# Performance work log

Measured on AMD Instinct MI355X. Metric: run time of the kernel, lower is better.

## Reference

```python
import jax, jax.numpy as jnp
import numpy as np

B, C, H, W = 128, 512, 14, 14
HEADS = 4
DH = C // HEADS  # 128
RH = RW = 7      # reduced KV grid (hardcoded 7x7 in source)
EPS = 1e-5
SCALE = DH ** -0.5


def _rel_pos_index():
    # replicates RelativePositionBias.__init__ index construction (h=w=7)
    coords = np.stack(np.meshgrid(np.arange(RH), np.arange(RW), indexing='ij'))
    cf = coords.reshape(2, -1)                       # [2,49]
    rc = cf[:, :, None] - cf[:, None, :]             # [2,49,49]
    rc = rc.transpose(1, 2, 0).copy()                # [49,49,2]
    rc[:, :, 0] += RH - 1
    rc[:, :, 1] += RW - 1
    rc[:, :, 0] *= 2 * RH - 1
    return rc.sum(-1)                                # [49,49] int

REL_IDX = _rel_pos_index()


def batchnorm(x, g, b, m, v):
    inv = g / jnp.sqrt(v + EPS)
    return x * inv[None, :, None, None] + (b - m * inv)[None, :, None, None]


def dsconv(x, w_dw, w_pw):
    # depthwise 3x3 (pad 1, groups=C) then pointwise 1x1, no bias
    cin = x.shape[1]
    y = jax.lax.conv_general_dilated(
        x, w_dw, window_strides=(1, 1), padding=((1, 1), (1, 1)),
        dimension_numbers=('NCHW', 'OIHW', 'NCHW'), feature_group_count=cin)
    return jnp.einsum('bchw,oc->bohw', y, w_pw)


def bilinear_to_7(x):
    # F.interpolate(size=(7,7), mode='bilinear', align_corners=True)
    hin, win = x.shape[2], x.shape[3]
    ys = jnp.linspace(0.0, hin - 1, RH)
    xs = jnp.linspace(0.0, win - 1, RW)
    y0 = jnp.floor(ys).astype(jnp.int32); y1 = jnp.minimum(y0 + 1, hin - 1)
    x0 = jnp.floor(xs).astype(jnp.int32); x1 = jnp.minimum(x0 + 1, win - 1)
    wy = (ys - y0)[:, None]                          # [7,1]
    wx = (xs - x0)[None, :]                          # [1,7]
    v00 = x[:, :, y0][:, :, :, x0]; v01 = x[:, :, y0][:, :, :, x1]
    v10 = x[:, :, y1][:, :, :, x0]; v11 = x[:, :, y1][:, :, :, x1]
    top = v00 * (1 - wx) + v01 * wx
    bot = v10 * (1 - wx) + v11 * wx
    return top * (1 - wy) + bot * wy


def _to_heads(t, h, w):
    # 'b (dim_head heads) h w -> b heads (h w) dim_head'
    b = t.shape[0]
    return jnp.transpose(t.reshape(b, DH, HEADS, h * w), (0, 2, 3, 1))


def setup_inputs() -> dict:
    key = jax.random.key(0)
    ks = jax.random.split(key, 16)
    p = {}
    p['x'] = jax.random.normal(ks[0], (B, C, H, W), jnp.float32)
    p['bn1_g'] = jax.random.normal(ks[1], (C,), jnp.float32) * 0.1 + 1.0
    p['bn1_b'] = jax.random.normal(ks[2], (C,), jnp.float32) * 0.1
    p['bn1_m'] = jax.random.normal(ks[3], (C,), jnp.float32) * 0.1
    p['bn1_v'] = jax.random.uniform(ks[4], (C,), jnp.float32, 0.5, 1.5)
    p['w_qkv_dw'] = jax.random.normal(ks[5], (C, 1, 3, 3), jnp.float32) * 0.1
    p['w_qkv_pw'] = jax.random.normal(ks[6], (3 * C, C), jnp.float32) * (C ** -0.5)
    p['rel_table'] = jax.random.normal(ks[7], ((2 * RH - 1) * (2 * RW - 1), HEADS), jnp.float32) * 0.02
    p['w_out_dw'] = jax.random.normal(ks[8], (C, 1, 3, 3), jnp.float32) * 0.1
    p['w_out_pw'] = jax.random.normal(ks[9], (C, C), jnp.float32) * (C ** -0.5)
    p['bn2_g'] = jax.random.normal(ks[10], (C,), jnp.float32) * 0.1 + 1.0
    p['bn2_b'] = jax.random.normal(ks[11], (C,), jnp.float32) * 0.1
    p['bn2_m'] = jax.random.normal(ks[12], (C,), jnp.float32) * 0.1
    p['bn2_v'] = jax.random.uniform(ks[13], (C,), jnp.float32, 0.5, 1.5)
    p['w_mlp'] = jax.random.normal(ks[14], (C, C), jnp.float32) * (C ** -0.5)
    return p


def reference(x, bn1_g, bn1_b, bn1_m, bn1_v, w_qkv_dw, w_qkv_pw, rel_table,
              w_out_dw, w_out_pw, bn2_g, bn2_b, bn2_m, bn2_v, w_mlp):
    out = batchnorm(x, bn1_g, bn1_b, bn1_m, bn1_v)
    qkv = dsconv(out, w_qkv_dw, w_qkv_pw)            # [B,3C,H,W]
    q, k, v = jnp.split(qkv, 3, axis=1)
    k = bilinear_to_7(k)
    v = bilinear_to_7(v)
    q = _to_heads(q, H, W)                           # [B,h,196,dh]
    k = _to_heads(k, RH, RW)                         # [B,h,49,dh]
    v = _to_heads(v, RH, RW)
    attn = jnp.einsum('bhid,bhjd->bhij', q, k)       # [B,h,196,49]
    # gathered relative-position bias, expanded 7x7 -> 14x14 via repeat_interleave
    bias = rel_table[REL_IDX.reshape(-1)].reshape(RH, RW, RH * RW, HEADS)
    bias = jnp.repeat(bias, 2, axis=0)
    bias = jnp.repeat(bias, 2, axis=1)               # [14,14,49,heads]
    bias = jnp.transpose(bias.reshape(H * W, RH * RW, HEADS), (2, 0, 1))[None]
    attn = (attn + bias) * SCALE                     # NOTE: scale applied after bias (faithful)
    attn = jax.nn.softmax(attn, axis=-1)
    o = jnp.einsum('bhij,bhjd->bhid', attn, v)       # [B,h,196,dh]
    o = jnp.transpose(o, (0, 3, 1, 2)).reshape(x.shape[0], C, H, W)
    o = dsconv(o, w_out_dw, w_out_pw)
    out = o + x
    residue = out
    out = batchnorm(out, bn2_g, bn2_b, bn2_m, bn2_v)
    out = jax.nn.relu(out)
    out = jnp.einsum('bchw,oc->bohw', out, w_mlp)
    return out + residue
```

## Files before the change

kernel.cpp:

```cpp
#include <hip/hip_runtime.h>

typedef short bf16x8 __attribute__((ext_vector_type(8)));
typedef float f32x4 __attribute__((ext_vector_type(4)));
typedef unsigned short u16;

#define ATT_SCALE 0.08838834764831845f

__device__ __forceinline__ u16 cvt_bf(float f) {
    union { float f; unsigned u; } a; a.f = f;
    unsigned r = a.u + 0x7FFFu + ((a.u >> 16) & 1u);
    return (u16)(r >> 16);
}

__device__ __forceinline__ float bf2f(u16 h) {
    union { unsigned u; float f; } a; a.u = ((unsigned)h) << 16;
    return a.f;
}

__device__ __forceinline__ void gload_lds16(const void* g, void* l) {
    __builtin_amdgcn_global_load_lds(
        (const __attribute__((address_space(1))) unsigned int*)g,
        (__attribute__((address_space(3))) unsigned int*)l, 16, 0, 0);
}

__global__ __launch_bounds__(256) void k0_prep(
    const float* __restrict__ wqkv, const float* __restrict__ wout,
    const float* __restrict__ wmlp,
    const float* __restrict__ g1, const float* __restrict__ b1,
    const float* __restrict__ m1, const float* __restrict__ v1,
    const float* __restrict__ g2, const float* __restrict__ b2,
    const float* __restrict__ m2, const float* __restrict__ v2,
    u16* __restrict__ W1p, u16* __restrict__ W2p, u16* __restrict__ W3p,
    float* __restrict__ s1, float* __restrict__ t1,
    float* __restrict__ s2, float* __restrict__ t2)
{
    int idx = blockIdx.x * 256 + threadIdx.x;
    if (idx < 786432) {
        int o = idx >> 9, c = idx & 511;
        int part = o >> 9, wi = o & 511;
        int hh = wi >> 7, dd = wi & 127;
        int orig = part * 512 + dd * 4 + hh;
        W1p[idx] = cvt_bf(wqkv[orig * 512 + c]);
    } else if (idx < 1048576) {
        int j = idx - 786432;
        int o = j >> 9, cp = j & 511;
        int oc = ((cp & 127) << 2) | (cp >> 7);
        W2p[j] = cvt_bf(wout[o * 512 + oc]);
    } else if (idx < 1310720) {
        int j = idx - 1048576;
        W3p[j] = cvt_bf(wmlp[j]);
    } else if (idx < 1311232) {
        int c = idx - 1310720;
        float i1 = g1[c] / sqrtf(v1[c] + 1e-5f);
        s1[c] = i1; t1[c] = b1[c] - m1[c] * i1;
        float i2 = g2[c] / sqrtf(v2[c] + 1e-5f);
        s2[c] = i2; t2[c] = b2[c] - m2[c] * i2;
    }
}

__global__ __launch_bounds__(256) void k1_bn_dw_bil(
    const float* __restrict__ x, const float* __restrict__ wdw,
    const float* __restrict__ s1, const float* __restrict__ t1,
    u16* __restrict__ ybf, u16* __restrict__ ybil)
{
    __shared__ u16 xs[32][199];
    __shared__ u16 ys[32][199];
    __shared__ float wt[32][9];
    __shared__ float sc[32], tc[32];
    int b = blockIdx.x >> 4, cg = blockIdx.x & 15;
    int c0 = cg * 32;
    int t = threadIdx.x;
    if (t < 32) { sc[t] = s1[c0 + t]; tc[t] = t1[c0 + t]; }
    for (int i = t; i < 288; i += 256) wt[i / 9][i % 9] = wdw[(c0 + i / 9) * 9 + i % 9];
    __syncthreads();
    const float4* xb4 = (const float4*)(x + ((size_t)b * 512 + c0) * 196);
    for (int i = t; i < 1568; i += 256) {
        int c = i / 49, j = i - c * 49;
        float4 v = xb4[i];
        float ss = sc[c], tt = tc[c];
        xs[c][4 * j]     = cvt_bf(v.x * ss + tt);
        xs[c][4 * j + 1] = cvt_bf(v.y * ss + tt);
        xs[c][4 * j + 2] = cvt_bf(v.z * ss + tt);
        xs[c][4 * j + 3] = cvt_bf(v.w * ss + tt);
    }
    __syncthreads();
    for (int i = t; i < 6272; i += 256) {
        int c = i & 31, p = i >> 5;
        int ii = p / 14, jj = p - ii * 14;
        float acc = 0.f;
        #pragma unroll
        for (int di = -1; di <= 1; ++di) {
            int i2 = ii + di;
            if (i2 < 0 || i2 > 13) continue;
            #pragma unroll
            for (int dj = -1; dj <= 1; ++dj) {
                int j2 = jj + dj;
                if (j2 < 0 || j2 > 13) continue;
                acc += wt[c][(di + 1) * 3 + (dj + 1)] * bf2f(xs[c][i2 * 14 + j2]);
            }
        }
        u16 ab = cvt_bf(acc);
        ys[c][p] = ab;
        ybf[((size_t)b * 196 + p) * 512 + c0 + c] = ab;
    }
    __syncthreads();
    for (int i = t; i < 1568; i += 256) {
        int c = i & 31, r = i >> 5;
        int ri = r / 7, rj = r - ri * 7;
        float fy = 13.f * ri / 6.f, fx = 13.f * rj / 6.f;
        int y0 = (int)fy; int y1 = min(y0 + 1, 13);
        int x0 = (int)fx; int x1 = min(x0 + 1, 13);
        float wy = fy - y0, wx = fx - x0;
        float v00 = bf2f(ys[c][y0 * 14 + x0]), v01 = bf2f(ys[c][y0 * 14 + x1]);
        float v10 = bf2f(ys[c][y1 * 14 + x0]), v11 = bf2f(ys[c][y1 * 14 + x1]);
        float top = v00 + (v01 - v00) * wx;
        float bot = v10 + (v11 - v10) * wx;
        float r7  = top + (bot - top) * wy;
        ybil[((size_t)b * 49 + r) * 512 + c0 + c] = cvt_bf(r7);
    }
}

template<int EPI>
__global__ __launch_bounds__(256, 2) void gemm_tn(
    const u16* __restrict__ A, const u16* __restrict__ Bw,
    float* __restrict__ out, int ldo,
    const float* __restrict__ auxf, u16* __restrict__ auxb,
    const float* __restrict__ s2, const float* __restrict__ t2)
{
    __shared__ __attribute__((aligned(16))) char smA[8192];
    __shared__ __attribute__((aligned(16))) char smB[8192];
    int t = threadIdx.x;
    int wv = t >> 6, l = t & 63;
    int wr = wv >> 1, wc = wv & 1;
    int m0 = blockIdx.x * 128, n0 = blockIdx.y * 128;
    f32x4 acc[4][4];
    #pragma unroll
    for (int mi = 0; mi < 4; ++mi)
        #pragma unroll
        for (int ni = 0; ni < 4; ++ni)
            acc[mi][ni] = f32x4{0.f, 0.f, 0.f, 0.f};

    const char* Ag = (const char*)A + (size_t)(m0 + (t >> 2)) * 1024 + ((t & 3) << 4);
    const char* Bg = (const char*)Bw + (size_t)(n0 + (t >> 2)) * 1024 + ((t & 3) << 4);
    char* lA = smA + wv * 1024;
    char* lB = smB + wv * 1024;
    int kb = (l >> 4) << 4;
    int rA = wr * 64 + (l & 15);
    int rB = wc * 64 + (l & 15);

    for (int kt = 0; kt < 16; ++kt) {
        __syncthreads();
        gload_lds16(Ag, lA);
        gload_lds16(Ag + 65536, lA + 4096);
        gload_lds16(Bg, lB);
        gload_lds16(Bg + 65536, lB + 4096);
        Ag += 64; Bg += 64;
        __syncthreads();
        bf16x8 af[4], bfr[4];
        #pragma unroll
        for (int mi = 0; mi < 4; ++mi)
            af[mi] = *(const bf16x8*)(smA + (rA + mi * 16) * 64 + kb);
        #pragma unroll
        for (int ni = 0; ni < 4; ++ni)
            bfr[ni] = *(const bf16x8*)(smB + (rB + ni * 16) * 64 + kb);
        #pragma unroll
        for (int mi = 0; mi < 4; ++mi)
            #pragma unroll
            for (int ni = 0; ni < 4; ++ni)
                acc[mi][ni] = __builtin_amdgcn_mfma_f32_16x16x32_bf16(af[mi], bfr[ni], acc[mi][ni], 0, 0, 0);
    }

    #pragma unroll
    for (int mi = 0; mi < 4; ++mi) {
        int rowg = m0 + wr * 64 + mi * 16 + ((l >> 4) << 2);
        if (EPI == 0) {
            #pragma unroll
            for (int ni = 0; ni < 4; ++ni) {
                int colg = n0 + wc * 64 + ni * 16 + (l & 15);
                float* op = out + (size_t)rowg * ldo + colg;
                #pragma unroll
                for (int v = 0; v < 4; ++v) op[(size_t)v * ldo] = acc[mi][ni][v];
            }
        } else if (EPI == 3) {
            #pragma unroll
            for (int ni = 0; ni < 4; ++ni) {
                int colg = n0 + wc * 64 + ni * 16 + (l & 15);
                #pragma unroll
                for (int v = 0; v < 4; ++v)
                    auxb[(size_t)(rowg + v) * ldo + colg] = cvt_bf(acc[mi][ni][v]);
            }
        } else if (EPI == 1) {
            int bb = rowg / 196, pp = rowg - bb * 196;
            #pragma unroll
            for (int ni = 0; ni < 4; ++ni) {
                int colg = n0 + wc * 64 + ni * 16 + (l & 15);
                float4 xv = *(const float4*)(auxf + (size_t)bb * 100352 + (size_t)colg * 196 + pp);
                const float* xa = (const float*)&xv;
                float ss = s2[colg], tt = t2[colg];
                #pragma unroll
                for (int v = 0; v < 4; ++v) {
                    float rv = acc[mi][ni][v] + xa[v];
                    out[(size_t)(rowg + v) * 512 + colg] = rv;
                    float av = rv * ss + tt;
                    av = av > 0.f ? av : 0.f;
                    auxb[(size_t)(rowg + v) * 512 + colg] = cvt_bf(av);
                }
            }
        } else {
            int bb = rowg / 196, pp = rowg - bb * 196;
            #pragma unroll
            for (int ni = 0; ni < 4; ++ni) {
                int colg = n0 + wc * 64 + ni * 16 + (l & 15);
                float4 dv;
                float* da = (float*)&dv;
                #pragma unroll
                for (int v = 0; v < 4; ++v)
                    da[v] = acc[mi][ni][v] + auxf[(size_t)(rowg + v) * 512 + colg];
                *(float4*)(out + (size_t)bb * 100352 + (size_t)colg * 196 + pp) = dv;
            }
        }
    }
}

#define K4_KLS   0
#define K4_VT    16384
#define K4_BIAS  32768
#define K4_SHR   45312
__global__ __launch_bounds__(256) void k4_attn(
    const u16* __restrict__ qbf, const u16* __restrict__ kvbf,
    const float* __restrict__ rel, u16* __restrict__ O)
{
    __shared__ __attribute__((aligned(16))) char sm[61696];
    int b = blockIdx.x >> 2, h = blockIdx.x & 3;
    int t = threadIdx.x, w = t >> 6, l = t & 63;
    const char* kvbase = (const char*)(kvbf + (size_t)b * 49 * 1024 + h * 128);
    for (int id = t; id < 1024; id += 256) {
        int r = id >> 4, c = id & 15;
        uint4 kvv = make_uint4(0, 0, 0, 0), vvv = make_uint4(0, 0, 0, 0);
        if (r < 49) {
            kvv = *(const uint4*)(kvbase + (size_t)r * 2048 + c * 16);
            vvv = *(const uint4*)(kvbase + (size_t)r * 2048 + 1024 + c * 16);
        }
        *(uint4*)(sm + K4_KLS + r * 256 + ((c ^ (r & 15)) * 16)) = kvv;
        *(uint4*)(sm + K4_SHR + r * 256 + c * 16) = vvv;
    }
    float* bias7 = (float*)(sm + K4_BIAS);
    for (int id = t; id < 3136; id += 256) {
        int q7 = id >> 6, j = id & 63;
        float bv = -1e30f;
        if (j < 49) {
            int ki = j / 7, kj = j - ki * 7;
            int qi = q7 / 7, qj = q7 - qi * 7;
            bv = rel[((qi - ki + 6) * 13 + (qj - kj + 6)) * 4 + h];
        }
        bias7[id] = bv;
    }
    __syncthreads();
    for (int li = 0; li < 4; ++li) {
        int id = li * 256 + t;
        int d = id & 127, jc = id >> 7;
        u16 vals[8];
        #pragma unroll
        for (int i = 0; i < 8; ++i)
            vals[i] = *(const u16*)(sm + K4_SHR + (jc * 8 + i) * 256 + d * 2);
        *(uint4*)(sm + K4_VT + d * 128 + ((jc ^ (d & 7)) * 16)) = *(uint4*)vals;
    }
    __syncthreads();
    const u16* qb = qbf + (size_t)b * 196 * 512 + h * 128;
    u16* Ob = O + (size_t)b * 196 * 512 + h * 128;
    char* Pls = sm + K4_SHR + w * 2048;
    for (int mt = w; mt < 13; mt += 4) {
        int m0 = mt * 16;
        int pa = m0 + (l & 15);
        const u16* qrow = qb + (size_t)pa * 512 + ((l >> 4) << 3);
        bf16x8 qf[4];
        #pragma unroll
        for (int kk = 0; kk < 4; ++kk) {
            bf16x8 z = {0, 0, 0, 0, 0, 0, 0, 0};
            qf[kk] = (pa < 196) ? *(const bf16x8*)(qrow + kk * 32) : z;
        }
        f32x4 s[4];
        #pragma unroll
        for (int nt = 0; nt < 4; ++nt) s[nt] = f32x4{0.f, 0.f, 0.f, 0.f};
        #pragma unroll
        for (int kk = 0; kk < 4; ++kk)
            #pragma unroll
            for (int nt = 0; nt < 4; ++nt) {
                int row = nt * 16 + (l & 15);
                bf16x8 kf = *(const bf16x8*)(sm + K4_KLS + row * 256 + (((kk * 4 + (l >> 4)) ^ (row & 15)) * 16));
                s[nt] = __builtin_amdgcn_mfma_f32_16x16x32_bf16(qf[kk], kf, s[nt], 0, 0, 0);
            }
        asm volatile("s_waitcnt lgkmcnt(0)" ::: "memory");
        float inv[4];
        #pragma unroll
        for (int v = 0; v < 4; ++v) {
            int p = m0 + ((l >> 4) << 2) + v;
            int pc = p < 196 ? p : 195;
            int ih = pc / 14, iw = pc - ih * 14;
            int q7 = (ih >> 1) * 7 + (iw >> 1);
            float sv[4];
            float mx = -3.0e38f;
            #pragma unroll
            for (int nt = 0; nt < 4; ++nt) {
                sv[nt] = (s[nt][v] + bias7[q7 * 64 + nt * 16 + (l & 15)]) * ATT_SCALE;
                mx = fmaxf(mx, sv[nt]);
            }
            #pragma unroll
            for (int o = 8; o >= 1; o >>= 1) mx = fmaxf(mx, __shfl_xor(mx, o));
            float den = 0.f, e[4];
            #pragma unroll
            for (int nt = 0; nt < 4; ++nt) { e[nt] = __expf(sv[nt] - mx); den += e[nt]; }
            #pragma unroll
            for (int o = 8; o >= 1; o >>= 1) den += __shfl_xor(den, o);
            inv[v] = 1.f / den;
            int row = ((l >> 4) << 2) + v;
            #pragma unroll
            for (int nt = 0; nt < 4; ++nt) {
                int col = nt * 16 + (l & 15);
                *(u16*)(Pls + row * 128 + (((col >> 3) ^ (row & 7)) * 16) + ((col & 7) * 2)) = cvt_bf(e[nt]);
            }
        }
        asm volatile("s_waitcnt lgkmcnt(0)" ::: "memory");
        __builtin_amdgcn_sched_barrier(0);
        f32x4 o[8];
        #pragma unroll
        for (int nt2 = 0; nt2 < 8; ++nt2) o[nt2] = f32x4{0.f, 0.f, 0.f, 0.f};
        #pragma unroll
        for (int kk = 0; kk < 2; ++kk) {
            int rowp = l & 15;
            bf16x8 pf = *(const bf16x8*)(Pls + rowp * 128 + (((kk * 4 + (l >> 4)) ^ (rowp & 7)) * 16));
            #pragma unroll
            for (int nt2 = 0; nt2 < 8; ++nt2) {
                int d = nt2 * 16 + (l & 15);
                bf16x8 vf = *(const bf16x8*)(sm + K4_VT + d * 128 + (((kk * 4 + (l >> 4)) ^ (d & 7)) * 16));
                o[nt2] = __builtin_amdgcn_mfma_f32_16x16x32_bf16(pf, vf, o[nt2], 0, 0, 0);
            }
        }
        #pragma unroll
        for (int nt2 = 0; nt2 < 8; ++nt2) {
            #pragma unroll
            for (int v = 0; v < 4; ++v) {
                int p = m0 + ((l >> 4) << 2) + v;
                if (p < 196)
                    Ob[(size_t)p * 512 + nt2 * 16 + (l & 15)] = cvt_bf(o[nt2][v] * inv[v]);
            }
        }
    }
}

__global__ __launch_bounds__(256) void k5_dw2(
    const u16* __restrict__ O, const float* __restrict__ wdw,
    u16* __restrict__ z)
{
    __shared__ u16 xs[32][199];
    __shared__ float wt[32][9];
    int b = blockIdx.x >> 4, cg = blockIdx.x & 15;
    int c0 = cg * 32;
    int t = threadIdx.x;
    for (int i = t; i < 288; i += 256) {
        int cl = i / 9;
        int cp = c0 + cl;
        int corig = ((cp & 127) << 2) | (cp >> 7);
        wt[cl][i % 9] = wdw[corig * 9 + i % 9];
    }
    const u16* Ob = O + (size_t)b * 196 * 512 + c0;
    for (int i = t; i < 6272; i += 256) {
        int c = i & 31, p = i >> 5;
        xs[c][p] = Ob[(size_t)p * 512 + c];
    }
    __syncthreads();
    for (int i = t; i < 6272; i += 256) {
        int c = i & 31, p = i >> 5;
        int ii = p / 14, jj = p - ii * 14;
        float acc = 0.f;
        #pragma unroll
        for (int di = -1; di <= 1; ++di) {
            int i2 = ii + di;
            if (i2 < 0 || i2 > 13) continue;
            #pragma unroll
            for (int dj = -1; dj <= 1; ++dj) {
                int j2 = jj + dj;
                if (j2 < 0 || j2 > 13) continue;
                acc += wt[c][(di + 1) * 3 + (dj + 1)] * bf2f(xs[c][i2 * 14 + j2]);
            }
        }
        z[((size_t)b * 196 + p) * 512 + c0 + c] = cvt_bf(acc);
    }
}

extern "C" void kernel_launch(void* const* d_in, const int* in_sizes, int n_in,
                              void* d_out, int out_size, void* d_ws, size_t ws_size,
                              hipStream_t stream)
{
    const float* x    = (const float*)d_in[0];
    const float* g1   = (const float*)d_in[1];
    const float* b1   = (const float*)d_in[2];
    const float* m1   = (const float*)d_in[3];
    const float* v1   = (const float*)d_in[4];
    const float* wqdw = (const float*)d_in[5];
    const float* wqpw = (const float*)d_in[6];
    const float* rel  = (const float*)d_in[7];
    const float* wodw = (const float*)d_in[8];
    const float* wopw = (const float*)d_in[9];
    const float* g2   = (const float*)d_in[10];
    const float* b2   = (const float*)d_in[11];
    const float* m2   = (const float*)d_in[12];
    const float* v2   = (const float*)d_in[13];
    const float* wmlp = (const float*)d_in[14];

    char* ws = (char*)d_ws;
    size_t off = 0;
    auto alloc = [&](size_t bytes) { char* p = ws + off; off += (bytes + 255) & ~(size_t)255; return p; };
    u16* W1p  = (u16*)alloc(1536ull * 512 * 2);
    u16* W2p  = (u16*)alloc(512ull * 512 * 2);
    u16* W3p  = (u16*)alloc(512ull * 512 * 2);
    float* s1 = (float*)alloc(512 * 4);
    float* t1 = (float*)alloc(512 * 4);
    float* s2 = (float*)alloc(512 * 4);
    float* t2 = (float*)alloc(512 * 4);
    u16* ybf  = (u16*)alloc(25088ull * 512 * 2);
    u16* ybil = (u16*)alloc(6272ull * 512 * 2);
    float* qbuf = (float*)alloc(25088ull * 512 * 4);
    float* kv7  = (float*)alloc(6272ull * 1024 * 4);
    u16* Obuf = (u16*)alloc(25088ull * 512 * 2);
    (void)ws_size; (void)in_sizes; (void)n_in; (void)out_size;

    u16* qbf  = (u16*)qbuf;
    u16* kvbf = (u16*)kv7;

    k0_prep<<<5122, 256, 0, stream>>>(wqpw, wopw, wmlp, g1, b1, m1, v1, g2, b2, m2, v2,
                                      W1p, W2p, W3p, s1, t1, s2, t2);
    k1_bn_dw_bil<<<2048, 256, 0, stream>>>(x, wqdw, s1, t1, ybf, ybil);
    gemm_tn<3><<<dim3(196, 4), 256, 0, stream>>>(ybf, W1p, nullptr, 512, nullptr, qbf, nullptr, nullptr);
    gemm_tn<3><<<dim3(49, 8), 256, 0, stream>>>(ybil, W1p + 262144, nullptr, 1024, nullptr, kvbf, nullptr, nullptr);
    k4_attn<<<512, 256, 0, stream>>>(qbf, kvbf, rel, Obuf);
    u16* zbuf = (u16*)kv7;
    k5_dw2<<<2048, 256, 0, stream>>>(Obuf, wodw, zbuf);
    float* resid = qbuf;
    u16* abuf = ybf;
    gemm_tn<1><<<dim3(196, 4), 256, 0, stream>>>(zbuf, W2p, resid, 512, x, abuf, s2, t2);
    gemm_tn<2><<<dim3(196, 4), 256, 0, stream>>>(abuf, W3p, (float*)d_out, 512, resid, nullptr, nullptr, nullptr);
}
```

Before: 358.8 us.

## Restructure depthwise convs with padded LDS tiles and row-per-thread register sliding windows

```diff
diff --git a/kernel.cpp b/kernel.cpp
--- a/kernel.cpp
+++ b/kernel.cpp
@@ -58,61 +58,80 @@
     }
 }
 
-__global__ __launch_bounds__(256) void k1_bn_dw_bil(
+__global__ __launch_bounds__(448) void k1_bn_dw_bil(
     const float* __restrict__ x, const float* __restrict__ wdw,
     const float* __restrict__ s1, const float* __restrict__ t1,
     u16* __restrict__ ybf, u16* __restrict__ ybil)
 {
-    __shared__ u16 xs[32][199];
-    __shared__ u16 ys[32][199];
+    __shared__ __attribute__((aligned(16))) u16 xs[32 * 264];
+    __shared__ u16 ys[32 * 198];
     __shared__ float wt[32][9];
     __shared__ float sc[32], tc[32];
     int b = blockIdx.x >> 4, cg = blockIdx.x & 15;
     int c0 = cg * 32;
     int t = threadIdx.x;
     if (t < 32) { sc[t] = s1[c0 + t]; tc[t] = t1[c0 + t]; }
-    for (int i = t; i < 288; i += 256) wt[i / 9][i % 9] = wdw[(c0 + i / 9) * 9 + i % 9];
+    if (t < 288) wt[t / 9][t % 9] = wdw[(c0 + t / 9) * 9 + t % 9];
+    for (int i = t; i < 4224; i += 448) ((unsigned*)xs)[i] = 0;
     __syncthreads();
     const float4* xb4 = (const float4*)(x + ((size_t)b * 512 + c0) * 196);
-    for (int i = t; i < 1568; i += 256) {
-        int c = i / 49, j = i - c * 49;
+    for (int i = t; i < 1568; i += 448) {
+        int c = i / 49, j4 = i - c * 49;
         float4 v = xb4[i];
         float ss = sc[c], tt = tc[c];
-        xs[c][4 * j]     = cvt_bf(v.x * ss + tt);
-        xs[c][4 * j + 1] = cvt_bf(v.y * ss + tt);
-        xs[c][4 * j + 2] = cvt_bf(v.z * ss + tt);
-        xs[c][4 * j + 3] = cvt_bf(v.w * ss + tt);
-    }
-    __syncthreads();
-    for (int i = t; i < 6272; i += 256) {
+        float vv[4] = {v.x, v.y, v.z, v.w};
+        #pragma unroll
+        for (int k = 0; k < 4; ++k) {
+            int p = 4 * j4 + k;
+            int r = p / 14, jj = p - r * 14;
+            xs[c * 264 + (r + 1) * 16 + (jj + 1)] = cvt_bf(vv[k] * ss + tt);
+        }
+    }
+    __syncthreads();
+    {
+        int r = t >> 5, c = t & 31;
+        float rowf[3][16];
+        #pragma unroll
+        for (int dr = 0; dr < 3; ++dr) {
+            uint4 a0 = *(const uint4*)&xs[c * 264 + (r + dr) * 16];
+            uint4 a1 = *(const uint4*)&xs[c * 264 + (r + dr) * 16 + 8];
+            unsigned ua[8] = {a0.x, a0.y, a0.z, a0.w, a1.x, a1.y, a1.z, a1.w};
+            #pragma unroll
+            for (int q = 0; q < 8; ++q) {
+                union { unsigned u; float f; } lo, hi;
+                lo.u = ua[q] << 16; hi.u = ua[q] & 0xFFFF0000u;
+                rowf[dr][2 * q] = lo.f; rowf[dr][2 * q + 1] = hi.f;
+            }
+        }
+        float w[9];
+        #pragma unroll
+        for (int k = 0; k < 9; ++k) w[k] = wt[c][k];
+        #pragma unroll
+        for (int j = 0; j < 14; ++j) {
+            float acc = 0.f;
+            #pragma unroll
+            for (int dr = 0; dr < 3; ++dr)
+                #pragma unroll
+                for (int dc = 0; dc < 3; ++dc)
+                    acc += w[dr * 3 + dc] * rowf[dr][j + dc];
+            ys[c * 198 + r * 14 + j] = cvt_bf(acc);
+        }
+    }
+    __syncthreads();
+    u16* yb = ybf + (size_t)b * 196 * 512 + c0;
+    for (int i = t; i < 6272; i += 448) {
         int c = i & 31, p = i >> 5;
-        int ii = p / 14, jj = p - ii * 14;
-        float acc = 0.f;
-        #pragma unroll
-        for (int di = -1; di <= 1; ++di) {
-            int i2 = ii + di;
-            if (i2 < 0 || i2 > 13) continue;
-            #pragma unroll
-            for (int dj = -1; dj <= 1; ++dj) {
-                int j2 = jj + dj;
-                if (j2 < 0 || j2 > 13) continue;
-                acc += wt[c][(di + 1) * 3 + (dj + 1)] * bf2f(xs[c][i2 * 14 + j2]);
-            }
-        }
-        u16 ab = cvt_bf(acc);
-        ys[c][p] = ab;
-        ybf[((size_t)b * 196 + p) * 512 + c0 + c] = ab;
-    }
-    __syncthreads();
-    for (int i = t; i < 1568; i += 256) {
+        yb[(size_t)p * 512 + c] = ys[c * 198 + p];
+    }
+    for (int i = t; i < 1568; i += 448) {
         int c = i & 31, r = i >> 5;
         int ri = r / 7, rj = r - ri * 7;
         float fy = 13.f * ri / 6.f, fx = 13.f * rj / 6.f;
         int y0 = (int)fy; int y1 = min(y0 + 1, 13);
         int x0 = (int)fx; int x1 = min(x0 + 1, 13);
         float wy = fy - y0, wx = fx - x0;
-        float v00 = bf2f(ys[c][y0 * 14 + x0]), v01 = bf2f(ys[c][y0 * 14 + x1]);
-        float v10 = bf2f(ys[c][y1 * 14 + x0]), v11 = bf2f(ys[c][y1 * 14 + x1]);
+        float v00 = bf2f(ys[c * 198 + y0 * 14 + x0]), v01 = bf2f(ys[c * 198 + y0 * 14 + x1]);
+        float v10 = bf2f(ys[c * 198 + y1 * 14 + x0]), v11 = bf2f(ys[c * 198 + y1 * 14 + x1]);
         float top = v00 + (v01 - v00) * wx;
         float bot = v10 + (v11 - v10) * wx;
         float r7  = top + (bot - top) * wy;
@@ -348,43 +367,69 @@
     }
 }
 
-__global__ __launch_bounds__(256) void k5_dw2(
+__global__ __launch_bounds__(448) void k5_dw2(
     const u16* __restrict__ O, const float* __restrict__ wdw,
     u16* __restrict__ z)
 {
-    __shared__ u16 xs[32][199];
+    __shared__ __attribute__((aligned(16))) u16 xs[32 * 264];
+    __shared__ u16 ys[32 * 198];
     __shared__ float wt[32][9];
     int b = blockIdx.x >> 4, cg = blockIdx.x & 15;
     int c0 = cg * 32;
     int t = threadIdx.x;
-    for (int i = t; i < 288; i += 256) {
-        int cl = i / 9;
+    if (t < 288) {
+        int cl = t / 9;
         int cp = c0 + cl;
         int corig = ((cp & 127) << 2) | (cp >> 7);
-        wt[cl][i % 9] = wdw[corig * 9 + i % 9];
-    }
+        wt[cl][t % 9] = wdw[corig * 9 + t % 9];
+    }
+    for (int i = t; i < 4224; i += 448) ((unsigned*)xs)[i] = 0;
+    __syncthreads();
     const u16* Ob = O + (size_t)b * 196 * 512 + c0;
-    for (int i = t; i < 6272; i += 256) {
+    for (int i = t; i < 784; i += 448) {
+        int p = i >> 2, c8 = i & 3;
+        uint4 v = *(const uint4*)&Ob[(size_t)p * 512 + c8 * 8];
+        int r = p / 14, jj = p - r * 14;
+        u16 tmp[8]; *(uint4*)tmp = v;
+        #pragma unroll
+        for (int k = 0; k < 8; ++k)
+            xs[(c8 * 8 + k) * 264 + (r + 1) * 16 + (jj + 1)] = tmp[k];
+    }
+    __syncthreads();
+    {
+        int r = t >> 5, c = t & 31;
+        float rowf[3][16];
+        #pragma unroll
+        for (int dr = 0; dr < 3; ++dr) {
+            uint4 a0 = *(const uint4*)&xs[c * 264 + (r + dr) * 16];
+            uint4 a1 = *(const uint4*)&xs[c * 264 + (r + dr) * 16 + 8];
+            unsigned ua[8] = {a0.x, a0.y, a0.z, a0.w, a1.x, a1.y, a1.z, a1.w};
+            #pragma unroll
+            for (int q = 0; q < 8; ++q) {
+                union { unsigned u; float f; } lo, hi;
+                lo.u = ua[q] << 16; hi.u = ua[q] & 0xFFFF0000u;
+                rowf[dr][2 * q] = lo.f; rowf[dr][2 * q + 1] = hi.f;
+            }
+        }
+        float w[9];
+        #pragma unroll
+        for (int k = 0; k < 9; ++k) w[k] = wt[c][k];
+        #pragma unroll
+        for (int j = 0; j < 14; ++j) {
+            float acc = 0.f;
+            #pragma unroll
+            for (int dr = 0; dr < 3; ++dr)
+                #pragma unroll
+                for (int dc = 0; dc < 3; ++dc)
+                    acc += w[dr * 3 + dc] * rowf[dr][j + dc];
+            ys[c * 198 + r * 14 + j] = cvt_bf(acc);
+        }
+    }
+    __syncthreads();
+    u16* zb = z + (size_t)b * 196 * 512 + c0;
+    for (int i = t; i < 6272; i += 448) {
         int c = i & 31, p = i >> 5;
-        xs[c][p] = Ob[(size_t)p * 512 + c];
-    }
-    __syncthreads();
-    for (int i = t; i < 6272; i += 256) {
-        int c = i & 31, p = i >> 5;
-        int ii = p / 14, jj = p - ii * 14;
-        float acc = 0.f;
-        #pragma unroll
-        for (int di = -1; di <= 1; ++di) {
-            int i2 = ii + di;
-            if (i2 < 0 || i2 > 13) continue;
-            #pragma unroll
-            for (int dj = -1; dj <= 1; ++dj) {
-                int j2 = jj + dj;
-                if (j2 < 0 || j2 > 13) continue;
-                acc += wt[c][(di + 1) * 3 + (dj + 1)] * bf2f(xs[c][i2 * 14 + j2]);
-            }
-        }
-        z[((size_t)b * 196 + p) * 512 + c0 + c] = cvt_bf(acc);
+        zb[(size_t)p * 512 + c] = ys[c * 198 + p];
     }
 }
 
@@ -430,12 +475,12 @@
 
     k0_prep<<<5122, 256, 0, stream>>>(wqpw, wopw, wmlp, g1, b1, m1, v1, g2, b2, m2, v2,
                                       W1p, W2p, W3p, s1, t1, s2, t2);
-    k1_bn_dw_bil<<<2048, 256, 0, stream>>>(x, wqdw, s1, t1, ybf, ybil);
+    k1_bn_dw_bil<<<2048, 448, 0, stream>>>(x, wqdw, s1, t1, ybf, ybil);
     gemm_tn<3><<<dim3(196, 4), 256, 0, stream>>>(ybf, W1p, nullptr, 512, nullptr, qbf, nullptr, nullptr);
     gemm_tn<3><<<dim3(49, 8), 256, 0, stream>>>(ybil, W1p + 262144, nullptr, 1024, nullptr, kvbf, nullptr, nullptr);
     k4_attn<<<512, 256, 0, stream>>>(qbf, kvbf, rel, Obuf);
     u16* zbuf = (u16*)kv7;
-    k5_dw2<<<2048, 256, 0, stream>>>(Obuf, wodw, zbuf);
+    k5_dw2<<<2048, 448, 0, stream>>>(Obuf, wodw, zbuf);
     float* resid = qbuf;
     u16* abuf = ybf;
     gemm_tn<1><<<dim3(196, 4), 256, 0, stream>>>(zbuf, W2p, resid, 512, x, abuf, s2, t2);
```

After: 321.7 us. -10.3%, faster.
